# Kernel optimization log

Hardware: AMD Instinct MI355X
Metric: run time of the kernel (lower is better)

Reference implementation:

```python
import jax, jax.numpy as jnp
import numpy as np

# M5-style dims
N = 30490          # nodes (3049 items x 10 stores)
E = 487840         # edges (~16 avg degree)
T = 90             # time steps (largest signature window)
C = 2              # input channels
WINDOWS = (7, 28, 90)
H, DH, HID, L, ET = 4, 32, 128, 3, 3   # heads, head_dim, gat hidden, layers, edge types
HOR, NG = 28, 7
MAX_RATIO = 20.0
D_LL = 2 * C                                  # lead-lag channel count
SIG_PER_WIN = D_LL + D_LL**2 + D_LL**3        # depth-3 signature dim = 84
SIG_DIM = len(WINDOWS) * SIG_PER_WIN          # 252
EMB_DIM = 8 + 8 + 4 + 4 + 16                  # 40


def _lead_lag(x):
    # (N, T, C) -> (N, 2T-1, 2C) standard lead-lag path augmentation
    xr = jnp.repeat(x, 2, axis=1)
    return jnp.concatenate([xr[:, 1:, :], xr[:, :-1, :]], axis=-1)


def _sig3(path):
    # exact truncated (depth-3) path signature of a piecewise-linear path (N, M+1, d)
    dx = path[:, 1:] - path[:, :-1]                      # (N, M, d)
    n, _, d = dx.shape
    c1 = jnp.cumsum(dx, axis=1) - dx                     # exclusive cumsum: S1 before step i
    s1 = dx.sum(axis=1)                                  # (N, d)
    inc2 = c1[..., :, None] * dx[..., None, :] + 0.5 * dx[..., :, None] * dx[..., None, :]
    c2 = jnp.cumsum(inc2, axis=1) - inc2                 # exclusive S2 before step i (N,M,d,d)
    s2 = inc2.sum(axis=1)                                # (N, d, d)
    # Chen: S3 += S2<i (x) dx + S1<i (x) dx(x)dx / 2 + dx(x)dx(x)dx / 6
    s3 = (jnp.einsum('nmab,nmc->nabc', c2, dx)
          + 0.5 * jnp.einsum('nma,nmb,nmc->nabc', c1, dx, dx)
          + jnp.einsum('nma,nmb,nmc->nabc', dx, dx, dx) / 6.0)
    return jnp.concatenate([s1, s2.reshape(n, d * d), s3.reshape(n, d * d * d)], axis=-1)


def _signature_features(x):
    return jnp.concatenate([_sig3(_lead_lag(x[:, -w:, :])) for w in WINDOWS], axis=-1)


def _layer_norm(x, g, b):
    m = x.mean(axis=-1, keepdims=True)
    v = ((x - m) ** 2).mean(axis=-1, keepdims=True)
    return (x - m) / jnp.sqrt(v + 1e-5) * g + b


def _gat_layer(h, src, dst, etype, W, b, a_src, a_dst, et_bias, Wres):
    n = h.shape[0]
    q = (h @ W + b).reshape(n, H, DH)                    # (N, H, DH)
    es = (q * a_src).sum(-1)                             # (N, H)
    ed = (q * a_dst).sum(-1)
    logit = jax.nn.leaky_relu(es[src] + ed[dst] + et_bias[etype], 0.2)   # (E, H)
    m = jax.lax.stop_gradient(jax.ops.segment_max(logit, dst, num_segments=n))
    m = jnp.where(jnp.isfinite(m), m, 0.0)
    ex = jnp.exp(logit - m[dst])
    den = jax.ops.segment_sum(ex, dst, num_segments=n)
    alpha = ex / (den[dst] + 1e-9)                       # per-destination softmax
    msg = jax.ops.segment_sum(alpha[:, :, None] * q[src], dst, num_segments=n)
    return jax.nn.elu(msg.reshape(n, H * DH) + h @ Wres)  # residual


def _forward(fl, edge_index, edge_type, store_id, dept_id, cat_id, state_id, item_id, dept_ids):
    (node_features, historical_mean, emb_store, emb_dept, emb_cat, emb_state, emb_item,
     fusion_W, fusion_b, ln_g, ln_b, gat_W, gat_b, gat_asrc, gat_adst, gat_et, gat_Wres,
     pred_W1, pred_b1, pred_W2, pred_b2, pred_W3, pred_b3, horizon_scale, group_scale) = fl
    sig = _signature_features(node_features)             # (N, 252)
    cat = jnp.concatenate([emb_store[store_id], emb_dept[dept_id], emb_cat[cat_id],
                           emb_state[state_id], emb_item[item_id]], axis=-1)  # (N, 40)
    h = jnp.concatenate([sig, cat], axis=-1)
    h = _layer_norm(jax.nn.gelu(h @ fusion_W + fusion_b, approximate=False), ln_g, ln_b)
    src, dst = edge_index[0], edge_index[1]
    for i in range(L):
        h = _gat_layer(h, src, dst, edge_type, gat_W[i], gat_b[i],
                       gat_asrc[i], gat_adst[i], gat_et[i], gat_Wres[i])
    x = jax.nn.gelu(h @ pred_W1 + pred_b1, approximate=False)
    x = jax.nn.gelu(x @ pred_W2 + pred_b2, approximate=False)
    pred = (x @ pred_W3 + pred_b3) * jax.nn.softplus(horizon_scale)
    # simple reconciliation: per-group learnable scale + clip by historical mean
    pred = pred * jax.nn.softplus(group_scale)[dept_ids][:, None]
    pred = jnp.clip(pred, 0.0, MAX_RATIO * historical_mean[:, None])
    return pred


def setup_inputs() -> dict:
    keys = iter(jax.random.split(jax.random.key(0), 40))
    def nrm(shape, s=0.05):
        return jax.random.normal(next(keys), shape, jnp.float32) * s
    inp = {}
    inp['node_features'] = jax.random.normal(next(keys), (N, T, C), jnp.float32)
    inp['edge_index'] = jax.random.randint(next(keys), (2, E), 0, N)
    inp['edge_type'] = jax.random.randint(next(keys), (E,), 0, ET)
    inp['store_id'] = jax.random.randint(next(keys), (N,), 0, 10)
    inp['dept_id'] = jax.random.randint(next(keys), (N,), 0, 7)
    inp['cat_id'] = jax.random.randint(next(keys), (N,), 0, 3)
    inp['state_id'] = jax.random.randint(next(keys), (N,), 0, 3)
    inp['item_id'] = jax.random.randint(next(keys), (N,), 0, 3049)
    inp['dept_ids'] = jax.random.randint(next(keys), (N,), 0, NG)
    inp['historical_mean'] = jax.random.uniform(next(keys), (N,), jnp.float32)
    # parameters
    inp['emb_store'] = nrm((10, 8), 0.1)
    inp['emb_dept'] = nrm((7, 8), 0.1)
    inp['emb_cat'] = nrm((3, 4), 0.1)
    inp['emb_state'] = nrm((3, 4), 0.1)
    inp['emb_item'] = nrm((3049, 16), 0.1)
    inp['fusion_W'] = nrm((SIG_DIM + EMB_DIM, HID))
    inp['fusion_b'] = jnp.zeros((HID,), jnp.float32)
    inp['ln_g'] = jnp.ones((HID,), jnp.float32)
    inp['ln_b'] = jnp.zeros((HID,), jnp.float32)
    inp['gat_W'] = nrm((L, HID, HID))
    inp['gat_b'] = jnp.zeros((L, HID), jnp.float32)
    inp['gat_asrc'] = nrm((L, H, DH), 0.1)
    inp['gat_adst'] = nrm((L, H, DH), 0.1)
    inp['gat_et'] = nrm((L, ET, H), 0.1)
    inp['gat_Wres'] = nrm((L, HID, HID))
    inp['pred_W1'] = nrm((HID, 256))
    inp['pred_b1'] = jnp.zeros((256,), jnp.float32)
    inp['pred_W2'] = nrm((256, 256))
    inp['pred_b2'] = jnp.zeros((256,), jnp.float32)
    inp['pred_W3'] = nrm((256, HOR))
    inp['pred_b3'] = jnp.zeros((HOR,), jnp.float32)
    inp['horizon_scale'] = jnp.ones((HOR,), jnp.float32)
    inp['group_scale'] = jnp.ones((NG,), jnp.float32)
    return inp


def reference(node_features, edge_index, edge_type, store_id, dept_id, cat_id, state_id,
              item_id, dept_ids, historical_mean, emb_store, emb_dept, emb_cat, emb_state,
              emb_item, fusion_W, fusion_b, ln_g, ln_b, gat_W, gat_b, gat_asrc, gat_adst,
              gat_et, gat_Wres, pred_W1, pred_b1, pred_W2, pred_b2, pred_W3, pred_b3,
              horizon_scale, group_scale):
    fl = (node_features, historical_mean, emb_store, emb_dept, emb_cat, emb_state, emb_item,
          fusion_W, fusion_b, ln_g, ln_b, gat_W, gat_b, gat_asrc, gat_adst, gat_et, gat_Wres,
          pred_W1, pred_b1, pred_W2, pred_b2, pred_W3, pred_b3, horizon_scale, group_scale)
    return _forward(fl, edge_index, edge_type, store_id, dept_id, cat_id, state_id, item_id, dept_ids)
```

## Files before the change

kernel.cpp:

```cpp
#include <hip/hip_runtime.h>
#include <math.h>

#define HID 128
#define DHD 32
#define N_T 90

__device__ __forceinline__ float gelu_f(float x) {
    return 0.5f * x * (1.0f + erff(x * 0.70710678118654752f));
}
__device__ __forceinline__ float softplus_f(float x) {
    return fmaxf(x, 0.0f) + log1pf(expf(-fabsf(x)));
}

template<int P>
__device__ __forceinline__ void sig_substep(float c1[4], float c2[16], float s3[64],
                                            float d0, float d1) {
    float h00 = 0.5f * d0 * d0, h01 = 0.5f * d0 * d1, h11 = 0.5f * d1 * d1;
#pragma unroll
    for (int a = 0; a < 4; ++a) {
#pragma unroll
        for (int b = 0; b < 4; ++b) {
            float c2ab = c2[a * 4 + b];
            s3[a * 16 + b * 4 + P + 0] += c2ab * d0;
            s3[a * 16 + b * 4 + P + 1] += c2ab * d1;
        }
    }
#pragma unroll
    for (int a = 0; a < 4; ++a) {
        float c = c1[a];
        s3[a * 16 + (P + 0) * 4 + (P + 0)] += c * h00;
        s3[a * 16 + (P + 0) * 4 + (P + 1)] += c * h01;
        s3[a * 16 + (P + 1) * 4 + (P + 0)] += c * h01;
        s3[a * 16 + (P + 1) * 4 + (P + 1)] += c * h11;
    }
    const float i6 = 0.16666666666666666f;
    float t000 = d0 * d0 * d0 * i6, t001 = d0 * d0 * d1 * i6;
    float t011 = d0 * d1 * d1 * i6, t111 = d1 * d1 * d1 * i6;
    s3[(P + 0) * 16 + (P + 0) * 4 + (P + 0)] += t000;
    s3[(P + 0) * 16 + (P + 0) * 4 + (P + 1)] += t001;
    s3[(P + 0) * 16 + (P + 1) * 4 + (P + 0)] += t001;
    s3[(P + 0) * 16 + (P + 1) * 4 + (P + 1)] += t011;
    s3[(P + 1) * 16 + (P + 0) * 4 + (P + 0)] += t001;
    s3[(P + 1) * 16 + (P + 0) * 4 + (P + 1)] += t011;
    s3[(P + 1) * 16 + (P + 1) * 4 + (P + 0)] += t011;
    s3[(P + 1) * 16 + (P + 1) * 4 + (P + 1)] += t111;
#pragma unroll
    for (int a = 0; a < 4; ++a) {
        float c = c1[a];
        c2[a * 4 + P + 0] += c * d0;
        c2[a * 4 + P + 1] += c * d1;
    }
    c2[(P + 0) * 4 + (P + 0)] += h00;
    c2[(P + 0) * 4 + (P + 1)] += h01;
    c2[(P + 1) * 4 + (P + 0)] += h01;
    c2[(P + 1) * 4 + (P + 1)] += h11;
    c1[P + 0] += d0;
    c1[P + 1] += d1;
}

__global__ void sig_kernel(const float* __restrict__ nf, float* __restrict__ X, int nn) {
    int node = blockIdx.x * blockDim.x + threadIdx.x;
    int win = blockIdx.y;
    if (node >= nn) return;
    int w = (win == 0) ? 7 : (win == 1) ? 28 : 90;
    const float* xp = nf + (size_t)node * (N_T * 2) + (size_t)(N_T - w) * 2;
    float c1[4] = {0.f, 0.f, 0.f, 0.f};
    float c2[16] = {0.f};
    float s3[64] = {0.f};
    float p0 = xp[0], p1 = xp[1];
    for (int i = 1; i < w; ++i) {
        float n0 = xp[i * 2], n1 = xp[i * 2 + 1];
        float d0 = n0 - p0, d1 = n1 - p1;
        sig_substep<0>(c1, c2, s3, d0, d1);
        sig_substep<2>(c1, c2, s3, d0, d1);
        p0 = n0; p1 = n1;
    }
    float* o = X + (size_t)node * 292 + win * 84;
#pragma unroll
    for (int k = 0; k < 4; ++k) o[k] = c1[k];
#pragma unroll
    for (int k = 0; k < 16; ++k) o[4 + k] = c2[k];
#pragma unroll
    for (int k = 0; k < 64; ++k) o[20 + k] = s3[k];
}

__global__ void emb_kernel(float* __restrict__ X,
                           const int* __restrict__ store_id, const int* __restrict__ dept_id,
                           const int* __restrict__ cat_id, const int* __restrict__ state_id,
                           const int* __restrict__ item_id,
                           const float* __restrict__ e_store, const float* __restrict__ e_dept,
                           const float* __restrict__ e_cat, const float* __restrict__ e_state,
                           const float* __restrict__ e_item, int nn) {
    int n = blockIdx.x * blockDim.x + threadIdx.x;
    if (n >= nn) return;
    float* o = X + (size_t)n * 292 + 252;
    const float* p;
    p = e_store + store_id[n] * 8;
#pragma unroll
    for (int j = 0; j < 8; ++j) o[j] = p[j];
    p = e_dept + dept_id[n] * 8;
#pragma unroll
    for (int j = 0; j < 8; ++j) o[8 + j] = p[j];
    p = e_cat + cat_id[n] * 4;
#pragma unroll
    for (int j = 0; j < 4; ++j) o[16 + j] = p[j];
    p = e_state + state_id[n] * 4;
#pragma unroll
    for (int j = 0; j < 4; ++j) o[20 + j] = p[j];
    p = e_item + item_id[n] * 16;
#pragma unroll
    for (int j = 0; j < 16; ++j) o[24 + j] = p[j];
}

__global__ __launch_bounds__(256)
void gemm128_kernel(const float* __restrict__ A, const float* __restrict__ B,
                    const float* __restrict__ bias, float* __restrict__ C,
                    int M, int N, int K, int act) {
    __shared__ float As[16][132];
    __shared__ float Bs[16][68];
    int tid = threadIdx.x;
    int bm = blockIdx.x * 128;
    int bn = blockIdx.y * 64;
    int tx = tid & 15, ty = tid >> 4;
    int ar = tid >> 2, ac = (tid & 3) * 4;
    int br = tid >> 4, bc = (tid & 15) * 4;
    float acc[8][4] = {};
    for (int k0 = 0; k0 < K; k0 += 16) {
        float av0[4] = {0.f, 0.f, 0.f, 0.f};
        float av1[4] = {0.f, 0.f, 0.f, 0.f};
        float bv[4]  = {0.f, 0.f, 0.f, 0.f};
        int gc = k0 + ac;
        int r0 = bm + ar, r1 = bm + ar + 64;
        if (gc + 4 <= K) {
            if (r0 < M) {
                float4 v = *(const float4*)(A + (size_t)r0 * K + gc);
                av0[0] = v.x; av0[1] = v.y; av0[2] = v.z; av0[3] = v.w;
            }
            if (r1 < M) {
                float4 v = *(const float4*)(A + (size_t)r1 * K + gc);
                av1[0] = v.x; av1[1] = v.y; av1[2] = v.z; av1[3] = v.w;
            }
        } else {
            for (int u = 0; u < 4; ++u) {
                if (gc + u < K) {
                    if (r0 < M) av0[u] = A[(size_t)r0 * K + gc + u];
                    if (r1 < M) av1[u] = A[(size_t)r1 * K + gc + u];
                }
            }
        }
        int brow = k0 + br;
        if (brow < K) {
            int gcB = bn + bc;
            if (gcB + 4 <= N) {
                float4 v = *(const float4*)(B + (size_t)brow * N + gcB);
                bv[0] = v.x; bv[1] = v.y; bv[2] = v.z; bv[3] = v.w;
            } else {
                for (int u = 0; u < 4; ++u)
                    if (gcB + u < N) bv[u] = B[(size_t)brow * N + gcB + u];
            }
        }
        __syncthreads();
#pragma unroll
        for (int u = 0; u < 4; ++u) {
            As[ac + u][ar] = av0[u];
            As[ac + u][ar + 64] = av1[u];
        }
        *(float4*)&Bs[br][bc] = make_float4(bv[0], bv[1], bv[2], bv[3]);
        __syncthreads();
#pragma unroll
        for (int kk = 0; kk < 16; ++kk) {
            float4 a0 = *(const float4*)&As[kk][ty * 8];
            float4 a1 = *(const float4*)&As[kk][ty * 8 + 4];
            float4 b  = *(const float4*)&Bs[kk][tx * 4];
            float aa[8] = {a0.x, a0.y, a0.z, a0.w, a1.x, a1.y, a1.z, a1.w};
            float bb[4] = {b.x, b.y, b.z, b.w};
#pragma unroll
            for (int i = 0; i < 8; ++i)
#pragma unroll
                for (int j = 0; j < 4; ++j) acc[i][j] += aa[i] * bb[j];
        }
    }
#pragma unroll
    for (int i = 0; i < 8; ++i) {
        int row = bm + ty * 8 + i;
        if (row >= M) continue;
        int col0 = bn + tx * 4;
        float v[4];
#pragma unroll
        for (int j = 0; j < 4; ++j) {
            float x = acc[i][j];
            int col = col0 + j;
            if (col < N && bias) x += bias[col];
            if (act == 1) x = gelu_f(x);
            v[j] = x;
        }
        if (col0 + 4 <= N) {
            *(float4*)(C + (size_t)row * N + col0) = make_float4(v[0], v[1], v[2], v[3]);
        } else {
            for (int j = 0; j < 4; ++j)
                if (col0 + j < N) C[(size_t)row * N + col0 + j] = v[j];
        }
    }
}

__global__ __launch_bounds__(256)
void gemm_kernel(const float* __restrict__ A, const float* __restrict__ B,
                 const float* __restrict__ bias, float* __restrict__ C,
                 int M, int N, int K, int act) {
    __shared__ float As[16][68];
    __shared__ float Bs[16][68];
    int tid = threadIdx.x;
    int bm = blockIdx.x * 64;
    int bn = blockIdx.y * 64;
    int tx = tid & 15, ty = tid >> 4;
    int ar = tid >> 2, ac = (tid & 3) * 4;
    int br = tid >> 4, bc = (tid & 15) * 4;
    float acc[4][4] = {};
    for (int k0 = 0; k0 < K; k0 += 16) {
        float av[4] = {0.f, 0.f, 0.f, 0.f};
        int grow = bm + ar;
        if (grow < M) {
            int gc = k0 + ac;
            if (gc + 4 <= K) {
                const float4 v = *(const float4*)(A + (size_t)grow * K + gc);
                av[0] = v.x; av[1] = v.y; av[2] = v.z; av[3] = v.w;
            } else {
                for (int u = 0; u < 4; ++u)
                    if (gc + u < K) av[u] = A[(size_t)grow * K + gc + u];
            }
        }
        float bv[4] = {0.f, 0.f, 0.f, 0.f};
        int brow = k0 + br;
        if (brow < K) {
            int gc = bn + bc;
            if (gc + 4 <= N) {
                const float4 v = *(const float4*)(B + (size_t)brow * N + gc);
                bv[0] = v.x; bv[1] = v.y; bv[2] = v.z; bv[3] = v.w;
            } else {
                for (int u = 0; u < 4; ++u)
                    if (gc + u < N) bv[u] = B[(size_t)brow * N + gc + u];
            }
        }
        __syncthreads();
        As[ac + 0][ar] = av[0];
        As[ac + 1][ar] = av[1];
        As[ac + 2][ar] = av[2];
        As[ac + 3][ar] = av[3];
        *(float4*)&Bs[br][bc] = make_float4(bv[0], bv[1], bv[2], bv[3]);
        __syncthreads();
#pragma unroll
        for (int kk = 0; kk < 16; ++kk) {
            float4 a = *(const float4*)&As[kk][ty * 4];
            float4 b = *(const float4*)&Bs[kk][tx * 4];
            float aa[4] = {a.x, a.y, a.z, a.w};
            float bb[4] = {b.x, b.y, b.z, b.w};
#pragma unroll
            for (int i = 0; i < 4; ++i)
#pragma unroll
                for (int j = 0; j < 4; ++j) acc[i][j] += aa[i] * bb[j];
        }
    }
#pragma unroll
    for (int i = 0; i < 4; ++i) {
        int row = bm + ty * 4 + i;
        if (row >= M) continue;
        int col0 = bn + tx * 4;
        float v[4];
#pragma unroll
        for (int j = 0; j < 4; ++j) {
            float x = acc[i][j];
            int col = col0 + j;
            if (col < N && bias) x += bias[col];
            if (act == 1) x = gelu_f(x);
            v[j] = x;
        }
        if (col0 + 4 <= N) {
            *(float4*)(C + (size_t)row * N + col0) = make_float4(v[0], v[1], v[2], v[3]);
        } else {
            for (int j = 0; j < 4; ++j)
                if (col0 + j < N) C[(size_t)row * N + col0 + j] = v[j];
        }
    }
}

__global__ void gelu_ln_kernel(float* __restrict__ h, const float* __restrict__ g,
                               const float* __restrict__ b) {
    int row = blockIdx.x, t = threadIdx.x;
    float* hp = h + (size_t)row * HID;
    float x = gelu_f(hp[t]);
    __shared__ float red[2];
    float s = x;
#pragma unroll
    for (int off = 32; off > 0; off >>= 1) s += __shfl_xor(s, off);
    if ((t & 63) == 0) red[t >> 6] = s;
    __syncthreads();
    float mean = (red[0] + red[1]) * (1.0f / 128.0f);
    float d = x - mean;
    float vs = d * d;
    __syncthreads();
#pragma unroll
    for (int off = 32; off > 0; off >>= 1) vs += __shfl_xor(vs, off);
    if ((t & 63) == 0) red[t >> 6] = vs;
    __syncthreads();
    float var = (red[0] + red[1]) * (1.0f / 128.0f);
    hp[t] = d / sqrtf(var + 1e-5f) * g[t] + b[t];
}

__global__ void hist_kernel(const int* __restrict__ dst, int* __restrict__ deg, int e) {
    int i = blockIdx.x * blockDim.x + threadIdx.x;
    if (i < e) atomicAdd(&deg[dst[i]], 1);
}

__global__ void scan_kernel(const int* __restrict__ deg, int* __restrict__ row_start,
                            int* __restrict__ cursor, int n) {
    __shared__ int wsum[16];
    __shared__ int chunk_total;
    int t = threadIdx.x;
    int lane = t & 63, wv = t >> 6;
    int carry = 0;
    for (int base = 0; base < n; base += 8192) {
        int idx0 = base + t * 8;
        int v[8];
        int s = 0;
#pragma unroll
        for (int u = 0; u < 8; ++u) {
            int d = (idx0 + u < n) ? deg[idx0 + u] : 0;
            v[u] = s;
            s += d;
        }
        int ws = s;
#pragma unroll
        for (int off = 1; off < 64; off <<= 1) {
            int u2 = __shfl_up(ws, off);
            if (lane >= off) ws += u2;
        }
        if (lane == 63) wsum[wv] = ws;
        __syncthreads();
        if (t == 0) {
            int a = 0;
#pragma unroll
            for (int k = 0; k < 16; ++k) {
                int tmp = wsum[k];
                wsum[k] = a;
                a += tmp;
            }
            chunk_total = a;
        }
        __syncthreads();
        int excl = ws - s + wsum[wv] + carry;
#pragma unroll
        for (int u = 0; u < 8; ++u) {
            if (idx0 + u < n) {
                row_start[idx0 + u] = excl + v[u];
                cursor[idx0 + u] = excl + v[u];
            }
        }
        carry += chunk_total;
        __syncthreads();
    }
    if (t == 0) row_start[n] = carry;
}

__global__ void scatter_kernel(const int* __restrict__ src, const int* __restrict__ dst,
                               const int* __restrict__ et, int* __restrict__ cursor,
                               int* __restrict__ csr_src, int* __restrict__ csr_de, int e) {
    int i = blockIdx.x * blockDim.x + threadIdx.x;
    if (i < e) {
        int d = dst[i];
        int pos = atomicAdd(&cursor[d], 1);
        csr_src[pos] = src[i];
        csr_de[pos] = d | (et[i] << 20);
    }
}

__global__ void esed_kernel(const float* __restrict__ q, const float* __restrict__ asrc,
                            const float* __restrict__ adst, float* __restrict__ es,
                            float* __restrict__ ed, int nn) {
    int idx = blockIdx.x * blockDim.x + threadIdx.x;
    if (idx >= nn * 4) return;
    int n = idx >> 2, hh = idx & 3;
    const float* qp = q + (size_t)n * HID + hh * DHD;
    const float* ap = asrc + hh * DHD;
    const float* dp = adst + hh * DHD;
    float s = 0.f, d = 0.f;
#pragma unroll
    for (int k = 0; k < DHD; ++k) {
        float qv = qp[k];
        s += qv * ap[k];
        d += qv * dp[k];
    }
    es[idx] = s;
    ed[idx] = d;
}

__global__ void lg_kernel(const int* __restrict__ csr_src, const int* __restrict__ csr_de,
                          const float* __restrict__ es, const float* __restrict__ ed,
                          const float* __restrict__ etb, float* __restrict__ lg_csr, int e) {
    int pos = blockIdx.x * blockDim.x + threadIdx.x;
    if (pos >= e) return;
    int s = csr_src[pos];
    int de = csr_de[pos];
    int d = de & 0xFFFFF;
    int et = de >> 20;
    float4 esv = *(const float4*)(es + (size_t)s * 4);
    float4 edv = *(const float4*)(ed + (size_t)d * 4);
    float4 bv  = *(const float4*)(etb + (size_t)et * 4);
    float l0 = esv.x + edv.x + bv.x;
    float l1 = esv.y + edv.y + bv.y;
    float l2 = esv.z + edv.z + bv.z;
    float l3 = esv.w + edv.w + bv.w;
    l0 = l0 > 0.f ? l0 : 0.2f * l0;
    l1 = l1 > 0.f ? l1 : 0.2f * l1;
    l2 = l2 > 0.f ? l2 : 0.2f * l2;
    l3 = l3 > 0.f ? l3 : 0.2f * l3;
    *(float4*)(lg_csr + (size_t)pos * 4) = make_float4(l0, l1, l2, l3);
}

__global__ void mden_kernel(const float* __restrict__ lg_csr, const int* __restrict__ row_start,
                            float* __restrict__ m_arr, float* __restrict__ den_arr, int nn) {
    int idx = blockIdx.x * blockDim.x + threadIdx.x;
    if (idx >= nn * 4) return;
    int n = idx >> 2, hh = idx & 3;
    int e0 = row_start[n], e1 = row_start[n + 1];
    float m = -INFINITY;
    for (int e = e0; e < e1; ++e) m = fmaxf(m, lg_csr[(size_t)e * 4 + hh]);
    if (e0 == e1) m = 0.f;
    float den = 0.f;
    for (int e = e0; e < e1; ++e) den += expf(lg_csr[(size_t)e * 4 + hh] - m);
    m_arr[idx] = m;
    den_arr[idx] = den;
}

__global__ void alpha_kernel(float* __restrict__ lg_csr, const int* __restrict__ csr_de,
                             const float* __restrict__ m_arr, const float* __restrict__ den_arr,
                             int e) {
    int idx = blockIdx.x * blockDim.x + threadIdx.x;
    if (idx >= e * 4) return;
    int pos = idx >> 2, hh = idx & 3;
    int d = csr_de[pos] & 0xFFFFF;
    float a = expf(lg_csr[idx] - m_arr[(size_t)d * 4 + hh]) /
              (den_arr[(size_t)d * 4 + hh] + 1e-9f);
    lg_csr[idx] = a;
}

__global__ void gat_agg_kernel(const float* __restrict__ q, const float* __restrict__ r,
                               const float* __restrict__ alpha_csr,
                               const int* __restrict__ row_start, const int* __restrict__ csr_src,
                               float* __restrict__ hout, int nn) {
    int n = blockIdx.x;
    int t = threadIdx.x;
    int hh = t >> 5;
    int e0 = row_start[n], e1 = row_start[n + 1];
    float acc = 0.f;
    for (int e = e0; e < e1; ++e) {
        int s = csr_src[e];
        float al = alpha_csr[(size_t)e * 4 + hh];
        acc += al * q[(size_t)s * HID + t];
    }
    float v = acc + r[(size_t)n * HID + t];
    hout[(size_t)n * HID + t] = v > 0.f ? v : expm1f(v);
}

__global__ void final_kernel(const float* __restrict__ y, const float* __restrict__ hs,
                             const float* __restrict__ gs, const int* __restrict__ dept_ids,
                             const float* __restrict__ hm, float* __restrict__ out, int nn) {
    int idx = blockIdx.x * blockDim.x + threadIdx.x;
    if (idx >= nn * 28) return;
    int n = idx / 28, j = idx - n * 28;
    float v = y[idx] * softplus_f(hs[j]) * softplus_f(gs[dept_ids[n]]);
    float hi = 20.0f * hm[n];
    out[idx] = fminf(fmaxf(v, 0.0f), hi);
}

extern "C" void kernel_launch(void* const* d_in, const int* in_sizes, int n_in,
                              void* d_out, int out_size, void* d_ws, size_t ws_size,
                              hipStream_t stream) {
    const float* nf       = (const float*)d_in[0];
    const int*   eidx     = (const int*)d_in[1];
    const int*   etype    = (const int*)d_in[2];
    const int*   store_id = (const int*)d_in[3];
    const int*   dept_id  = (const int*)d_in[4];
    const int*   cat_id   = (const int*)d_in[5];
    const int*   state_id = (const int*)d_in[6];
    const int*   item_id  = (const int*)d_in[7];
    const int*   dept_ids = (const int*)d_in[8];
    const float* hm       = (const float*)d_in[9];
    const float* e_store  = (const float*)d_in[10];
    const float* e_dept   = (const float*)d_in[11];
    const float* e_cat    = (const float*)d_in[12];
    const float* e_state  = (const float*)d_in[13];
    const float* e_item   = (const float*)d_in[14];
    const float* fusion_W = (const float*)d_in[15];
    const float* fusion_b = (const float*)d_in[16];
    const float* ln_g     = (const float*)d_in[17];
    const float* ln_b     = (const float*)d_in[18];
    const float* gat_W    = (const float*)d_in[19];
    const float* gat_b    = (const float*)d_in[20];
    const float* gat_asrc = (const float*)d_in[21];
    const float* gat_adst = (const float*)d_in[22];
    const float* gat_et   = (const float*)d_in[23];
    const float* gat_Wres = (const float*)d_in[24];
    const float* pW1      = (const float*)d_in[25];
    const float* pb1      = (const float*)d_in[26];
    const float* pW2      = (const float*)d_in[27];
    const float* pb2      = (const float*)d_in[28];
    const float* pW3      = (const float*)d_in[29];
    const float* pb3      = (const float*)d_in[30];
    const float* hs       = (const float*)d_in[31];
    const float* gs       = (const float*)d_in[32];

    const int nn = in_sizes[3];
    const int ee = in_sizes[2];
    const int* src = eidx;
    const int* dst = eidx + ee;

    float* ws = (float*)d_ws;
    float* X   = ws;
    float* h   = X + (size_t)nn * 292;
    float* q   = h + (size_t)nn * 128;
    float* r   = q + (size_t)nn * 128;
    float* t2  = r + (size_t)nn * 128;
    float* es  = t2 + (size_t)nn * 256;
    float* ed  = es + (size_t)nn * 4;
    float* m_a = ed + (size_t)nn * 4;
    float* d_a = m_a + (size_t)nn * 4;
    float* lg  = d_a + (size_t)nn * 4;
    int* deg       = (int*)(lg + (size_t)ee * 4);
    int* row_start = deg + nn;
    int* cursor    = row_start + nn + 1;
    int* csr_src   = cursor + nn;
    int* csr_de    = csr_src + ee;
    float* t1 = X;
    float* y  = q;

    hipMemsetAsync(deg, 0, nn * sizeof(int), stream);
    hist_kernel<<<(ee + 255) / 256, 256, 0, stream>>>(dst, deg, ee);
    scan_kernel<<<1, 1024, 0, stream>>>(deg, row_start, cursor, nn);
    scatter_kernel<<<(ee + 255) / 256, 256, 0, stream>>>(src, dst, etype, cursor,
                                                         csr_src, csr_de, ee);

    dim3 sg((nn + 255) / 256, 3);
    sig_kernel<<<sg, 256, 0, stream>>>(nf, X, nn);
    emb_kernel<<<(nn + 255) / 256, 256, 0, stream>>>(X, store_id, dept_id, cat_id, state_id,
                                                     item_id, e_store, e_dept, e_cat, e_state,
                                                     e_item, nn);

    dim3 g128_2((nn + 127) / 128, 2);
    gemm128_kernel<<<g128_2, 256, 0, stream>>>(X, fusion_W, fusion_b, h, nn, 128, 292, 0);
    gelu_ln_kernel<<<nn, 128, 0, stream>>>(h, ln_g, ln_b);

    for (int l = 0; l < 3; ++l) {
        gemm128_kernel<<<g128_2, 256, 0, stream>>>(h, gat_W + (size_t)l * 128 * 128,
                                                   gat_b + l * 128, q, nn, 128, 128, 0);
        gemm128_kernel<<<g128_2, 256, 0, stream>>>(h, gat_Wres + (size_t)l * 128 * 128,
                                                   nullptr, r, nn, 128, 128, 0);
        esed_kernel<<<(nn * 4 + 255) / 256, 256, 0, stream>>>(q, gat_asrc + l * 128,
                                                              gat_adst + l * 128, es, ed, nn);
        lg_kernel<<<(ee + 255) / 256, 256, 0, stream>>>(csr_src, csr_de, es, ed,
                                                        gat_et + l * 12, lg, ee);
        mden_kernel<<<(nn * 4 + 255) / 256, 256, 0, stream>>>(lg, row_start, m_a, d_a, nn);
        alpha_kernel<<<(ee * 4 + 255) / 256, 256, 0, stream>>>(lg, csr_de, m_a, d_a, ee);
        gat_agg_kernel<<<nn, 128, 0, stream>>>(q, r, lg, row_start, csr_src, h, nn);
    }

    dim3 g128_4((nn + 127) / 128, 4);
    gemm128_kernel<<<g128_4, 256, 0, stream>>>(h, pW1, pb1, t1, nn, 256, 128, 1);
    gemm128_kernel<<<g128_4, 256, 0, stream>>>(t1, pW2, pb2, t2, nn, 256, 256, 1);
    dim3 g3((nn + 63) / 64, 1);
    gemm_kernel<<<g3, 256, 0, stream>>>(t2, pW3, pb3, y, nn, 28, 256, 0);
    final_kernel<<<(nn * 28 + 255) / 256, 256, 0, stream>>>(y, hs, gs, dept_ids, hm,
                                                            (float*)d_out, nn);
}
```

Measured before the change: 926.2 us.

## Replace GEMM kernels with double-buffered 64x128 tile GEMM and merge q/res projections

Replaces the two SGEMM kernels with one register-prefetched, double-buffered shared-memory GEMM that uses 64x128 output tiles and a K-step of 32, which cuts the barriers per tile to one. The kernel can also serve two weight matrices that share the same A in a single launch, so the GAT q and residual projections now run together. This is meant to overlap global loads with FMA work and to remove a launch per layer. It uses more shared memory (about 51KB), which may lower occupancy, and the N=28 final layer wastes most of its 128-wide tile.

```diff
diff --git a/kernel.cpp b/kernel.cpp
--- a/kernel.cpp
+++ b/kernel.cpp
@@ -113,171 +113,120 @@
 }
 
 __global__ __launch_bounds__(256)
-void gemm128_kernel(const float* __restrict__ A, const float* __restrict__ B,
-                    const float* __restrict__ bias, float* __restrict__ C,
-                    int M, int N, int K, int act) {
-    __shared__ float As[16][132];
-    __shared__ float Bs[16][68];
-    int tid = threadIdx.x;
-    int bm = blockIdx.x * 128;
-    int bn = blockIdx.y * 64;
-    int tx = tid & 15, ty = tid >> 4;
-    int ar = tid >> 2, ac = (tid & 3) * 4;
-    int br = tid >> 4, bc = (tid & 15) * 4;
-    float acc[8][4] = {};
-    for (int k0 = 0; k0 < K; k0 += 16) {
-        float av0[4] = {0.f, 0.f, 0.f, 0.f};
-        float av1[4] = {0.f, 0.f, 0.f, 0.f};
-        float bv[4]  = {0.f, 0.f, 0.f, 0.f};
-        int gc = k0 + ac;
-        int r0 = bm + ar, r1 = bm + ar + 64;
-        if (gc + 4 <= K) {
-            if (r0 < M) {
-                float4 v = *(const float4*)(A + (size_t)r0 * K + gc);
-                av0[0] = v.x; av0[1] = v.y; av0[2] = v.z; av0[3] = v.w;
-            }
-            if (r1 < M) {
-                float4 v = *(const float4*)(A + (size_t)r1 * K + gc);
-                av1[0] = v.x; av1[1] = v.y; av1[2] = v.z; av1[3] = v.w;
-            }
-        } else {
-            for (int u = 0; u < 4; ++u) {
-                if (gc + u < K) {
-                    if (r0 < M) av0[u] = A[(size_t)r0 * K + gc + u];
-                    if (r1 < M) av1[u] = A[(size_t)r1 * K + gc + u];
-                }
-            }
-        }
-        int brow = k0 + br;
-        if (brow < K) {
-            int gcB = bn + bc;
-            if (gcB + 4 <= N) {
-                float4 v = *(const float4*)(B + (size_t)brow * N + gcB);
-                bv[0] = v.x; bv[1] = v.y; bv[2] = v.z; bv[3] = v.w;
-            } else {
-                for (int u = 0; u < 4; ++u)
-                    if (gcB + u < N) bv[u] = B[(size_t)brow * N + gcB + u];
-            }
-        }
-        __syncthreads();
-#pragma unroll
-        for (int u = 0; u < 4; ++u) {
-            As[ac + u][ar] = av0[u];
-            As[ac + u][ar + 64] = av1[u];
-        }
-        *(float4*)&Bs[br][bc] = make_float4(bv[0], bv[1], bv[2], bv[3]);
-        __syncthreads();
-#pragma unroll
-        for (int kk = 0; kk < 16; ++kk) {
-            float4 a0 = *(const float4*)&As[kk][ty * 8];
-            float4 a1 = *(const float4*)&As[kk][ty * 8 + 4];
-            float4 b  = *(const float4*)&Bs[kk][tx * 4];
-            float aa[8] = {a0.x, a0.y, a0.z, a0.w, a1.x, a1.y, a1.z, a1.w};
-            float bb[4] = {b.x, b.y, b.z, b.w};
-#pragma unroll
-            for (int i = 0; i < 8; ++i)
-#pragma unroll
-                for (int j = 0; j < 4; ++j) acc[i][j] += aa[i] * bb[j];
-        }
-    }
-#pragma unroll
-    for (int i = 0; i < 8; ++i) {
-        int row = bm + ty * 8 + i;
-        if (row >= M) continue;
-        int col0 = bn + tx * 4;
-        float v[4];
-#pragma unroll
-        for (int j = 0; j < 4; ++j) {
-            float x = acc[i][j];
-            int col = col0 + j;
-            if (col < N && bias) x += bias[col];
-            if (act == 1) x = gelu_f(x);
-            v[j] = x;
-        }
-        if (col0 + 4 <= N) {
-            *(float4*)(C + (size_t)row * N + col0) = make_float4(v[0], v[1], v[2], v[3]);
-        } else {
-            for (int j = 0; j < 4; ++j)
-                if (col0 + j < N) C[(size_t)row * N + col0 + j] = v[j];
-        }
-    }
-}
-
-__global__ __launch_bounds__(256)
-void gemm_kernel(const float* __restrict__ A, const float* __restrict__ B,
-                 const float* __restrict__ bias, float* __restrict__ C,
-                 int M, int N, int K, int act) {
-    __shared__ float As[16][68];
-    __shared__ float Bs[16][68];
+void gemm_db_kernel(const float* __restrict__ A, int M, int K,
+                    const float* __restrict__ B1, const float* __restrict__ bias1,
+                    float* __restrict__ C1, int N1, int act1, int nby1,
+                    const float* __restrict__ B2, const float* __restrict__ bias2,
+                    float* __restrict__ C2, int N2, int act2) {
+    __shared__ float As[2][32][68];
+    __shared__ float Bs[2][32][132];
     int tid = threadIdx.x;
     int bm = blockIdx.x * 64;
-    int bn = blockIdx.y * 64;
+    int by = blockIdx.y;
+
+    const float* B = B1; const float* bias = bias1; float* C = C1;
+    int N = N1, act = act1, colbase;
+    if (by < nby1) {
+        colbase = by * 128;
+    } else {
+        B = B2; bias = bias2; C = C2; N = N2; act = act2;
+        colbase = (by - nby1) * 128;
+    }
+
+    int arow = tid >> 3;
+    int akq  = (tid & 7) * 4;
+    int bk   = tid >> 5;
+    int bnq  = (tid & 31) * 4;
     int tx = tid & 15, ty = tid >> 4;
-    int ar = tid >> 2, ac = (tid & 3) * 4;
-    int br = tid >> 4, bc = (tid & 15) * 4;
-    float acc[4][4] = {};
-    for (int k0 = 0; k0 < K; k0 += 16) {
-        float av[4] = {0.f, 0.f, 0.f, 0.f};
-        int grow = bm + ar;
-        if (grow < M) {
-            int gc = k0 + ac;
-            if (gc + 4 <= K) {
-                const float4 v = *(const float4*)(A + (size_t)grow * K + gc);
-                av[0] = v.x; av[1] = v.y; av[2] = v.z; av[3] = v.w;
+
+    float areg[2][4];
+    float breg[4][4];
+    float acc[4][8] = {};
+
+    int T = (K + 31) / 32;
+
+    auto load_tile = [&](int t) {
+        int k0 = t * 32;
+#pragma unroll
+        for (int i = 0; i < 2; ++i) {
+            int row = bm + arow + i * 32;
+            int col = k0 + akq;
+            if (row < M && col + 4 <= K) {
+                float4 v = *(const float4*)(A + (size_t)row * K + col);
+                areg[i][0] = v.x; areg[i][1] = v.y; areg[i][2] = v.z; areg[i][3] = v.w;
             } else {
+#pragma unroll
                 for (int u = 0; u < 4; ++u)
-                    if (gc + u < K) av[u] = A[(size_t)grow * K + gc + u];
+                    areg[i][u] = (row < M && col + u < K) ? A[(size_t)row * K + col + u] : 0.f;
             }
         }
-        float bv[4] = {0.f, 0.f, 0.f, 0.f};
-        int brow = k0 + br;
-        if (brow < K) {
-            int gc = bn + bc;
-            if (gc + 4 <= N) {
-                const float4 v = *(const float4*)(B + (size_t)brow * N + gc);
-                bv[0] = v.x; bv[1] = v.y; bv[2] = v.z; bv[3] = v.w;
+#pragma unroll
+        for (int i = 0; i < 4; ++i) {
+            int krow = k0 + bk + i * 8;
+            int col = colbase + bnq;
+            if (krow < K && col + 4 <= N) {
+                float4 v = *(const float4*)(B + (size_t)krow * N + col);
+                breg[i][0] = v.x; breg[i][1] = v.y; breg[i][2] = v.z; breg[i][3] = v.w;
             } else {
+#pragma unroll
                 for (int u = 0; u < 4; ++u)
-                    if (gc + u < N) bv[u] = B[(size_t)brow * N + gc + u];
+                    breg[i][u] = (krow < K && col + u < N) ? B[(size_t)krow * N + col + u] : 0.f;
             }
         }
+    };
+
+    auto store_tile = [&](int d) {
+#pragma unroll
+        for (int i = 0; i < 2; ++i)
+#pragma unroll
+            for (int u = 0; u < 4; ++u)
+                As[d][akq + u][arow + i * 32] = areg[i][u];
+#pragma unroll
+        for (int i = 0; i < 4; ++i)
+            *(float4*)&Bs[d][bk + i * 8][bnq] = make_float4(breg[i][0], breg[i][1],
+                                                            breg[i][2], breg[i][3]);
+    };
+
+    load_tile(0);
+    for (int t = 0; t < T; ++t) {
+        int d = t & 1;
+        store_tile(d);
+        if (t + 1 < T) load_tile(t + 1);
         __syncthreads();
-        As[ac + 0][ar] = av[0];
-        As[ac + 1][ar] = av[1];
-        As[ac + 2][ar] = av[2];
-        As[ac + 3][ar] = av[3];
-        *(float4*)&Bs[br][bc] = make_float4(bv[0], bv[1], bv[2], bv[3]);
-        __syncthreads();
-#pragma unroll
-        for (int kk = 0; kk < 16; ++kk) {
-            float4 a = *(const float4*)&As[kk][ty * 4];
-            float4 b = *(const float4*)&Bs[kk][tx * 4];
+#pragma unroll
+        for (int kk = 0; kk < 32; ++kk) {
+            float4 a = *(const float4*)&As[d][kk][ty * 4];
+            float4 b0 = *(const float4*)&Bs[d][kk][tx * 8];
+            float4 b1 = *(const float4*)&Bs[d][kk][tx * 8 + 4];
             float aa[4] = {a.x, a.y, a.z, a.w};
-            float bb[4] = {b.x, b.y, b.z, b.w};
+            float bb[8] = {b0.x, b0.y, b0.z, b0.w, b1.x, b1.y, b1.z, b1.w};
 #pragma unroll
             for (int i = 0; i < 4; ++i)
 #pragma unroll
-                for (int j = 0; j < 4; ++j) acc[i][j] += aa[i] * bb[j];
-        }
-    }
+                for (int j = 0; j < 8; ++j) acc[i][j] += aa[i] * bb[j];
+        }
+    }
+
 #pragma unroll
     for (int i = 0; i < 4; ++i) {
         int row = bm + ty * 4 + i;
         if (row >= M) continue;
-        int col0 = bn + tx * 4;
-        float v[4];
-#pragma unroll
-        for (int j = 0; j < 4; ++j) {
+        int col0 = colbase + tx * 8;
+        float v[8];
+#pragma unroll
+        for (int j = 0; j < 8; ++j) {
             float x = acc[i][j];
             int col = col0 + j;
-            if (col < N && bias) x += bias[col];
+            if (bias && col < N) x += bias[col];
             if (act == 1) x = gelu_f(x);
             v[j] = x;
         }
-        if (col0 + 4 <= N) {
+        if (col0 + 8 <= N) {
             *(float4*)(C + (size_t)row * N + col0) = make_float4(v[0], v[1], v[2], v[3]);
+            *(float4*)(C + (size_t)row * N + col0 + 4) = make_float4(v[4], v[5], v[6], v[7]);
         } else {
-            for (int j = 0; j < 4; ++j)
+#pragma unroll
+            for (int j = 0; j < 8; ++j)
                 if (col0 + j < N) C[(size_t)row * N + col0 + j] = v[j];
         }
     }
@@ -533,6 +482,8 @@
     float* t1 = X;
     float* y  = q;
 
+    const int gx = (nn + 63) / 64;
+
     hipMemsetAsync(deg, 0, nn * sizeof(int), stream);
     hist_kernel<<<(ee + 255) / 256, 256, 0, stream>>>(dst, deg, ee);
     scan_kernel<<<1, 1024, 0, stream>>>(deg, row_start, cursor, nn);
@@ -545,15 +496,16 @@
                                                      item_id, e_store, e_dept, e_cat, e_state,
                                                      e_item, nn);
 
-    dim3 g128_2((nn + 127) / 128, 2);
-    gemm128_kernel<<<g128_2, 256, 0, stream>>>(X, fusion_W, fusion_b, h, nn, 128, 292, 0);
+    gemm_db_kernel<<<dim3(gx, 1), 256, 0, stream>>>(
+        X, nn, 292, fusion_W, fusion_b, h, 128, 0, 1,
+        nullptr, nullptr, nullptr, 0, 0);
     gelu_ln_kernel<<<nn, 128, 0, stream>>>(h, ln_g, ln_b);
 
     for (int l = 0; l < 3; ++l) {
-        gemm128_kernel<<<g128_2, 256, 0, stream>>>(h, gat_W + (size_t)l * 128 * 128,
-                                                   gat_b + l * 128, q, nn, 128, 128, 0);
-        gemm128_kernel<<<g128_2, 256, 0, stream>>>(h, gat_Wres + (size_t)l * 128 * 128,
-                                                   nullptr, r, nn, 128, 128, 0);
+        gemm_db_kernel<<<dim3(gx, 2), 256, 0, stream>>>(
+            h, nn, 128,
+            gat_W + (size_t)l * 128 * 128, gat_b + l * 128, q, 128, 0, 1,
+            gat_Wres + (size_t)l * 128 * 128, nullptr, r, 128, 0);
         esed_kernel<<<(nn * 4 + 255) / 256, 256, 0, stream>>>(q, gat_asrc + l * 128,
                                                               gat_adst + l * 128, es, ed, nn);
         lg_kernel<<<(ee + 255) / 256, 256, 0, stream>>>(csr_src, csr_de, es, ed,
@@ -563,11 +515,15 @@
         gat_agg_kernel<<<nn, 128, 0, stream>>>(q, r, lg, row_start, csr_src, h, nn);
     }
 
-    dim3 g128_4((nn + 127) / 128, 4);
-    gemm128_kernel<<<g128_4, 256, 0, stream>>>(h, pW1, pb1, t1, nn, 256, 128, 1);
-    gemm128_kernel<<<g128_4, 256, 0, stream>>>(t1, pW2, pb2, t2, nn, 256, 256, 1);
-    dim3 g3((nn + 63) / 64, 1);
-    gemm_kernel<<<g3, 256, 0, stream>>>(t2, pW3, pb3, y, nn, 28, 256, 0);
+    gemm_db_kernel<<<dim3(gx, 2), 256, 0, stream>>>(
+        h, nn, 128, pW1, pb1, t1, 256, 1, 2,
+        nullptr, nullptr, nullptr, 0, 0);
+    gemm_db_kernel<<<dim3(gx, 2), 256, 0, stream>>>(
+        t1, nn, 256, pW2, pb2, t2, 256, 1, 2,
+        nullptr, nullptr, nullptr, 0, 0);
+    gemm_db_kernel<<<dim3(gx, 1), 256, 0, stream>>>(
+        t2, nn, 256, pW3, pb3, y, 28, 0, 1,
+        nullptr, nullptr, nullptr, 0, 0);
     final_kernel<<<(nn * 28 + 255) / 256, 256, 0, stream>>>(y, hs, gs, dept_ids, hm,
                                                             (float*)d_out, nn);
 }
```

Result: slower. 974.2 us (+5.2%).
